# Kernel optimization log

Measured on AMD Instinct MI355X. Metric: run time of the kernel, lower is better.

The kernel has to match this reference:

```python
import jax, jax.numpy as jnp
import numpy as np

S, D, DD, REL, R = 4096, 128, 64, 8, 512
FC_IN = DD * (REL * S + R)  # 2,129,920


def setup_inputs() -> dict:
    key = jax.random.key(0)
    ks = jax.random.split(key, 7)
    return {
        "inputs": jax.random.randint(ks[0], (S,), 0, 2, dtype=jnp.int32),
        "rule_features": jax.random.normal(ks[1], (DD, R), dtype=jnp.float32),
        "embed_w": jax.random.normal(ks[2], (S, D), dtype=jnp.float32),
        "rel_w": jax.random.normal(ks[3], (REL, D), dtype=jnp.float32),
        "dise_w": jax.random.normal(ks[4], (DD, D), dtype=jnp.float32),
        "fc_w": jax.random.normal(ks[5], (DD, FC_IN), dtype=jnp.float32) * 0.01,
        "fc_b": jax.random.normal(ks[6], (DD,), dtype=jnp.float32),
    }


def reference(inputs, rule_features, embed_w, rel_w, dise_w, fc_w, fc_b):
    eps = 1e-6
    dt = embed_w.dtype
    # mask rows where the symptom indicator is nonzero (original builds mask
    # row-by-row with torch.nonzero; equivalent to broadcasting inputs != 0)
    mask = (inputs != 0).astype(dt)                                  # [S]
    # (embed + rel) * mask  -> [S, REL, D] -> [S*REL, D]
    x = (embed_w[:, None, :] + rel_w[None, :, :]) * mask[:, None, None]
    x = x.reshape(-1, embed_w.shape[-1])                             # [N, D]
    # cosine similarity of every disease embedding vs every (sym,rel) vector
    sq = jnp.sum(x * x, axis=1)                                      # [N]
    xn = jnp.where(sq > 0, jnp.sqrt(jnp.where(sq > 0, sq, 1.0)), 0.0)
    dn = jnp.sqrt(jnp.sum(dise_w * dise_w, axis=1))                  # [DD]
    dots = jnp.einsum('kd,nd->kn', dise_w, x)                        # [DD, N]
    kg = dots / jnp.maximum(dn[:, None] * xn[None, :], eps)          # [DD, N]
    hidden = jnp.concatenate([rule_features, kg], axis=1).reshape(1, -1)
    out = jax.nn.sigmoid(hidden @ fc_w.T + fc_b)                     # [1, DD]
    return out
```

## Files before the change

kernel.cpp:

```cpp
#include <hip/hip_runtime.h>
#include <math.h>

namespace {
constexpr int S_N   = 4096;
constexpr int D_N   = 128;
constexpr int DD_N  = 64;
constexpr int REL_N = 8;
constexpr int R_N   = 512;
constexpr int NTOT  = S_N * REL_N;
constexpr int ROWLEN = R_N + NTOT;
constexpr long long FC_IN_N = (long long)DD_N * ROWLEN;
constexpr int NCH   = 32;
constexpr int CHUNK2 = (int)(FC_IN_N / NCH);
constexpr int RPB   = 4;
constexpr int KG_N  = DD_N / RPB;
constexpr int NBLK3 = NCH * KG_N;
typedef float floatx4 __attribute__((ext_vector_type(4)));

__device__ __forceinline__ float dot4(const float4& a, const float4& b) {
    return a.x*b.x + a.y*b.y + a.z*b.z + a.w*b.w;
}
}

__global__ __launch_bounds__(256) void k_pre1(const float* __restrict__ dise,
                                              const float* __restrict__ embed,
                                              const float* __restrict__ rel,
                                              float* __restrict__ DE,
                                              float* __restrict__ DR,
                                              float* __restrict__ dsc_g) {
    __shared__ float sd[DD_N * 129];
    __shared__ __align__(16) float se[64 * D_N];
    __shared__ __align__(16) float sr[REL_N * D_N];
    const int tid  = threadIdx.x;
    const int lane = tid & 63;
    const int wave = tid >> 6;
    const int s0   = blockIdx.x * 64;

    for (int i = tid; i < DD_N * D_N; i += 256)
        sd[(i >> 7) * 129 + (i & 127)] = dise[i];
    for (int i = tid; i < 64 * D_N / 4; i += 256)
        reinterpret_cast<float4*>(se)[i] =
            reinterpret_cast<const float4*>(embed + (size_t)s0 * D_N)[i];
    if (tid < REL_N * D_N / 4)
        reinterpret_cast<float4*>(sr)[tid] = reinterpret_cast<const float4*>(rel)[tid];
    __syncthreads();

    float dw[D_N];
    float dsq = 0.f;
    #pragma unroll
    for (int e = 0; e < D_N; ++e) {
        dw[e] = sd[lane * 129 + e];
        dsq += dw[e] * dw[e];
    }
    const float dsc = rsqrtf(dsq);

    if (blockIdx.x == 0) {
        if (wave == 0) dsc_g[lane] = dsc;
        #pragma unroll
        for (int rr = 0; rr < 2; ++rr) {
            const int r = wave * 2 + rr;
            float a = 0.f;
            #pragma unroll
            for (int e = 0; e < D_N; ++e) a += dw[e] * sr[r * D_N + e];
            DR[lane * REL_N + r] = a;
        }
    }

    float* dst = DE + (size_t)lane * S_N + s0 + wave * 16;
    #pragma unroll
    for (int j4 = 0; j4 < 4; ++j4) {
        float4 o;
        float* op = reinterpret_cast<float*>(&o);
        #pragma unroll
        for (int jj = 0; jj < 4; ++jj) {
            const int nl = wave * 16 + j4 * 4 + jj;
            const float4* xr = reinterpret_cast<const float4*>(&se[nl * D_N]);
            float a0 = 0.f, a1 = 0.f, a2 = 0.f, a3 = 0.f;
            #pragma unroll
            for (int i = 0; i < 32; i += 4) {
                float4 x0 = xr[i], x1 = xr[i + 1], x2 = xr[i + 2], x3 = xr[i + 3];
                a0 += dw[4*i+ 0]*x0.x + dw[4*i+ 1]*x0.y + dw[4*i+ 2]*x0.z + dw[4*i+ 3]*x0.w;
                a1 += dw[4*i+ 4]*x1.x + dw[4*i+ 5]*x1.y + dw[4*i+ 6]*x1.z + dw[4*i+ 7]*x1.w;
                a2 += dw[4*i+ 8]*x2.x + dw[4*i+ 9]*x2.y + dw[4*i+10]*x2.z + dw[4*i+11]*x2.w;
                a3 += dw[4*i+12]*x3.x + dw[4*i+13]*x3.y + dw[4*i+14]*x3.z + dw[4*i+15]*x3.w;
            }
            op[jj] = a0 + a1 + a2 + a3;
        }
        *reinterpret_cast<float4*>(dst + j4 * 4) = o;
    }
}

__global__ __launch_bounds__(256) void k_pre0(const int* __restrict__ inputs,
                                              const float* __restrict__ embed,
                                              const float* __restrict__ rel,
                                              float* __restrict__ xinv) {
    __shared__ __align__(16) float sr[REL_N * D_N];
    __shared__ float rr[REL_N];
    const int tid = threadIdx.x;
    const int p  = tid & 3;
    const int sl = tid >> 2;
    const int s  = blockIdx.x * 64 + sl;

    if (tid < REL_N * D_N / 4)
        reinterpret_cast<float4*>(sr)[tid] = reinterpret_cast<const float4*>(rel)[tid];
    __syncthreads();
    if (tid < REL_N) {
        float a = 0.f;
        for (int e = 0; e < D_N; ++e) { float v = sr[tid * D_N + e]; a += v * v; }
        rr[tid] = a;
    }
    __syncthreads();

    float4 e4[8];
    const float4* ep = reinterpret_cast<const float4*>(embed + (size_t)s * D_N + p * 32);
    #pragma unroll
    for (int i = 0; i < 8; ++i) e4[i] = ep[i];
    float ee = 0.f;
    #pragma unroll
    for (int i = 0; i < 8; ++i) ee += dot4(e4[i], e4[i]);

    const float4* sr4 = reinterpret_cast<const float4*>(sr);
    float er[8];
    #pragma unroll
    for (int r = 0; r < REL_N; ++r) {
        float a = 0.f;
        #pragma unroll
        for (int i = 0; i < 8; ++i) a += dot4(e4[i], sr4[r * 32 + p * 8 + i]);
        er[r] = a;
    }

    ee += __shfl_xor(ee, 1); ee += __shfl_xor(ee, 2);
    #pragma unroll
    for (int r = 0; r < REL_N; ++r) {
        er[r] += __shfl_xor(er[r], 1);
        er[r] += __shfl_xor(er[r], 2);
    }

    if (p == 0) {
        const bool m = (inputs[s] != 0);
        float vr[8];
        #pragma unroll
        for (int r = 0; r < REL_N; ++r) {
            float sq = ee + 2.f * er[r] + rr[r];
            vr[r] = (m && sq > 0.f) ? rsqrtf(sq) : 0.f;
        }
        float4 o0, o1;
        o0.x = vr[0]; o0.y = vr[1]; o0.z = vr[2]; o0.w = vr[3];
        o1.x = vr[4]; o1.y = vr[5]; o1.z = vr[6]; o1.w = vr[7];
        float4* xp = reinterpret_cast<float4*>(xinv + (size_t)s * REL_N);
        xp[0] = o0; xp[1] = o1;
    }
}

__global__ __launch_bounds__(256) void k_kg2(const float* __restrict__ rf,
                                             const float* __restrict__ DE,
                                             const float* __restrict__ DR,
                                             const float* __restrict__ dsc_g,
                                             const float* __restrict__ xinv,
                                             float* __restrict__ h) {
    __shared__ __align__(16) float sx[8192];
    __shared__ float sD[1024];
    const int tid = threadIdx.x;
    const int dd  = blockIdx.x >> 2;
    const int q   = blockIdx.x & 3;
    const int n0  = q * 8192;
    const int s0  = q * 1024;

    for (int i = tid; i < 2048; i += 256)
        reinterpret_cast<float4*>(sx)[i] = reinterpret_cast<const float4*>(xinv + n0)[i];
    if (tid < 256)
        reinterpret_cast<float4*>(sD)[tid] =
            reinterpret_cast<const float4*>(DE + (size_t)dd * S_N + s0)[tid];
    const float dsc = dsc_g[dd];
    const float4 drlo = reinterpret_cast<const float4*>(DR + dd * REL_N)[0];
    const float4 drhi = reinterpret_cast<const float4*>(DR + dd * REL_N)[1];
    const float4 drv = (tid & 1) ? drhi : drlo;
    __syncthreads();

    float* hb = h + (size_t)dd * ROWLEN + R_N + n0;
    #pragma unroll
    for (int i = 0; i < 8; ++i) {
        const int f4i = i * 256 + tid;
        const int ln  = f4i * 4;
        const float de = sD[f4i >> 1];
        float4 xv = reinterpret_cast<const float4*>(sx)[f4i];
        float4 o;
        o.x = dsc * xv.x * (de + drv.x);
        o.y = dsc * xv.y * (de + drv.y);
        o.z = dsc * xv.z * (de + drv.z);
        o.w = dsc * xv.w * (de + drv.w);
        *reinterpret_cast<float4*>(hb + ln) = o;
    }
    if (q == 0 && tid < 128)
        reinterpret_cast<float4*>(h + (size_t)dd * ROWLEN)[tid] =
            reinterpret_cast<const float4*>(rf + (size_t)dd * R_N)[tid];
}

__global__ __launch_bounds__(256, 2) void k_mv(const float* __restrict__ fcw,
                                               const float* __restrict__ h,
                                               float* __restrict__ partials) {
    const int tid = threadIdx.x;
    const int swz = (blockIdx.x & 7) * (NBLK3 / 8) + (blockIdx.x >> 3);
    const int c  = swz >> 4;
    const int kg = swz & 15;

    const float4* hp = reinterpret_cast<const float4*>(h) + (size_t)c * (CHUNK2 / 4);
    const size_t wbase = (size_t)(kg * RPB) * (FC_IN_N / 4) + (size_t)c * (CHUNK2 / 4);
    const floatx4* wp0 = reinterpret_cast<const floatx4*>(fcw) + wbase;
    const floatx4* wp1 = wp0 + (FC_IN_N / 4);
    const floatx4* wp2 = wp1 + (FC_IN_N / 4);
    const floatx4* wp3 = wp2 + (FC_IN_N / 4);

    float a0 = 0.f, a1 = 0.f, a2 = 0.f, a3 = 0.f;
    #pragma unroll 5
    for (int i = 0; i < CHUNK2 / 4 / 256; ++i) {
        const int idx = i * 256 + tid;
        floatx4 w0 = __builtin_nontemporal_load(wp0 + idx);
        floatx4 w1 = __builtin_nontemporal_load(wp1 + idx);
        floatx4 w2 = __builtin_nontemporal_load(wp2 + idx);
        floatx4 w3 = __builtin_nontemporal_load(wp3 + idx);
        float4 hv = hp[idx];
        a0 += w0.x * hv.x + w0.y * hv.y + w0.z * hv.z + w0.w * hv.w;
        a1 += w1.x * hv.x + w1.y * hv.y + w1.z * hv.z + w1.w * hv.w;
        a2 += w2.x * hv.x + w2.y * hv.y + w2.z * hv.z + w2.w * hv.w;
        a3 += w3.x * hv.x + w3.y * hv.y + w3.z * hv.z + w3.w * hv.w;
    }

    #pragma unroll
    for (int m = 32; m >= 1; m >>= 1) {
        a0 += __shfl_xor(a0, m);
        a1 += __shfl_xor(a1, m);
        a2 += __shfl_xor(a2, m);
        a3 += __shfl_xor(a3, m);
    }
    __shared__ float red[4][RPB];
    if ((tid & 63) == 0) {
        const int wv = tid >> 6;
        red[wv][0] = a0; red[wv][1] = a1; red[wv][2] = a2; red[wv][3] = a3;
    }
    __syncthreads();
    if (tid < RPB) {
        partials[(size_t)swz * RPB + tid] =
            red[0][tid] + red[1][tid] + red[2][tid] + red[3][tid];
    }
}

__global__ __launch_bounds__(256) void k_fin(const float* __restrict__ partials,
                                             const float* __restrict__ fcb,
                                             float* __restrict__ out) {
    const int tid = threadIdx.x;
    const int k = tid & 63, g = tid >> 6;
    float s = 0.f;
    for (int b = g; b < NCH; b += 4) s += partials[(size_t)b * 64 + k];
    __shared__ float red[4][64];
    red[g][k] = s;
    __syncthreads();
    if (tid < 64) {
        float t = red[0][tid] + red[1][tid] + red[2][tid] + red[3][tid] + fcb[tid];
        out[tid] = 1.0f / (1.0f + expf(-t));
    }
}

extern "C" void kernel_launch(void* const* d_in, const int* in_sizes, int n_in,
                              void* d_out, int out_size, void* d_ws, size_t ws_size,
                              hipStream_t stream) {
    const int*   inputs = (const int*)  d_in[0];
    const float* rf     = (const float*)d_in[1];
    const float* embed  = (const float*)d_in[2];
    const float* rel    = (const float*)d_in[3];
    const float* dise   = (const float*)d_in[4];
    const float* fcw    = (const float*)d_in[5];
    const float* fcb    = (const float*)d_in[6];
    float* out = (float*)d_out;

    float* ws = (float*)d_ws;
    float* h        = ws;
    float* partials = h + FC_IN_N;
    float* DE       = partials + NCH * 64;
    float* DR       = DE + (size_t)DD_N * S_N;
    float* dsc_g    = DR + DD_N * REL_N;
    float* xinv     = dsc_g + 64;

    hipLaunchKernelGGL(k_pre1, dim3(S_N / 64), dim3(256), 0, stream, dise, embed, rel, DE, DR, dsc_g);
    hipLaunchKernelGGL(k_pre0, dim3(S_N / 64), dim3(256), 0, stream, inputs, embed, rel, xinv);
    hipLaunchKernelGGL(k_kg2,  dim3(DD_N * 4), dim3(256), 0, stream, rf, DE, DR, dsc_g, xinv, h);
    hipLaunchKernelGGL(k_mv,   dim3(NBLK3),    dim3(256), 0, stream, fcw, h, partials);
    hipLaunchKernelGGL(k_fin,  dim3(1),        dim3(256), 0, stream, partials, fcb, out);
}
```

Measured before the change: 117.9 us.

## Fuse preprocessing kernels and widen matvec blocks to eight rows

Merges the two preprocessing kernels into one that computes both the disease-embedding dot products and the inverse norms from the same shared tile. It uses 16 symptoms per block, giving four times as many blocks, and pads the shared rows to avoid bank conflicts. The fc matvec now uses 512-thread blocks that each handle 8 output rows, so every h load is reused across twice as many weight rows and there are half as many blocks. The trade-off is higher register pressure and fewer resident blocks in the dominant bandwidth-bound kernel, which could reduce memory-level parallelism.

```diff
diff --git a/kernel.cpp b/kernel.cpp
--- a/kernel.cpp
+++ b/kernel.cpp
@@ -12,9 +12,11 @@
 constexpr long long FC_IN_N = (long long)DD_N * ROWLEN;
 constexpr int NCH   = 32;
 constexpr int CHUNK2 = (int)(FC_IN_N / NCH);
-constexpr int RPB   = 4;
+constexpr int NF4   = CHUNK2 / 4;
+constexpr int RPB   = 8;
 constexpr int KG_N  = DD_N / RPB;
 constexpr int NBLK3 = NCH * KG_N;
+constexpr int SEP   = 132;
 typedef float floatx4 __attribute__((ext_vector_type(4)));
 
 __device__ __forceinline__ float dot4(const float4& a, const float4& b) {
@@ -22,28 +24,42 @@
 }
 }
 
-__global__ __launch_bounds__(256) void k_pre1(const float* __restrict__ dise,
-                                              const float* __restrict__ embed,
-                                              const float* __restrict__ rel,
-                                              float* __restrict__ DE,
-                                              float* __restrict__ DR,
-                                              float* __restrict__ dsc_g) {
+__global__ __launch_bounds__(256) void k_pre(const int* __restrict__ inputs,
+                                             const float* __restrict__ dise,
+                                             const float* __restrict__ embed,
+                                             const float* __restrict__ rel,
+                                             float* __restrict__ DE,
+                                             float* __restrict__ DR,
+                                             float* __restrict__ dsc_g,
+                                             float* __restrict__ xinv) {
     __shared__ float sd[DD_N * 129];
-    __shared__ __align__(16) float se[64 * D_N];
-    __shared__ __align__(16) float sr[REL_N * D_N];
+    __shared__ __align__(16) float se[16 * SEP];
+    __shared__ __align__(16) float sr[REL_N * SEP];
+    __shared__ float rr[REL_N];
     const int tid  = threadIdx.x;
     const int lane = tid & 63;
     const int wave = tid >> 6;
-    const int s0   = blockIdx.x * 64;
+    const int s0   = blockIdx.x * 16;
 
     for (int i = tid; i < DD_N * D_N; i += 256)
         sd[(i >> 7) * 129 + (i & 127)] = dise[i];
-    for (int i = tid; i < 64 * D_N / 4; i += 256)
-        reinterpret_cast<float4*>(se)[i] =
+    for (int i = tid; i < 16 * 32; i += 256) {
+        const int row = i >> 5, col = i & 31;
+        *reinterpret_cast<float4*>(&se[row * SEP + col * 4]) =
             reinterpret_cast<const float4*>(embed + (size_t)s0 * D_N)[i];
-    if (tid < REL_N * D_N / 4)
-        reinterpret_cast<float4*>(sr)[tid] = reinterpret_cast<const float4*>(rel)[tid];
-    __syncthreads();
+    }
+    if (tid < REL_N * 32) {
+        const int row = tid >> 5, col = tid & 31;
+        *reinterpret_cast<float4*>(&sr[row * SEP + col * 4]) =
+            reinterpret_cast<const float4*>(rel)[tid];
+    }
+    __syncthreads();
+
+    if (tid < REL_N) {
+        float a = 0.f;
+        for (int e = 0; e < D_N; ++e) { float v = sr[tid * SEP + e]; a += v * v; }
+        rr[tid] = a;
+    }
 
     float dw[D_N];
     float dsq = 0.f;
@@ -57,24 +73,22 @@
     if (blockIdx.x == 0) {
         if (wave == 0) dsc_g[lane] = dsc;
         #pragma unroll
-        for (int rr = 0; rr < 2; ++rr) {
-            const int r = wave * 2 + rr;
+        for (int rr2 = 0; rr2 < 2; ++rr2) {
+            const int r = wave * 2 + rr2;
             float a = 0.f;
             #pragma unroll
-            for (int e = 0; e < D_N; ++e) a += dw[e] * sr[r * D_N + e];
+            for (int e = 0; e < D_N; ++e) a += dw[e] * sr[r * SEP + e];
             DR[lane * REL_N + r] = a;
         }
     }
 
-    float* dst = DE + (size_t)lane * S_N + s0 + wave * 16;
-    #pragma unroll
-    for (int j4 = 0; j4 < 4; ++j4) {
+    {
         float4 o;
         float* op = reinterpret_cast<float*>(&o);
         #pragma unroll
         for (int jj = 0; jj < 4; ++jj) {
-            const int nl = wave * 16 + j4 * 4 + jj;
-            const float4* xr = reinterpret_cast<const float4*>(&se[nl * D_N]);
+            const int nl = wave * 4 + jj;
+            const float4* xr = reinterpret_cast<const float4*>(&se[nl * SEP]);
             float a0 = 0.f, a1 = 0.f, a2 = 0.f, a3 = 0.f;
             #pragma unroll
             for (int i = 0; i < 32; i += 4) {
@@ -86,69 +100,25 @@
             }
             op[jj] = a0 + a1 + a2 + a3;
         }
-        *reinterpret_cast<float4*>(dst + j4 * 4) = o;
-    }
-}
-
-__global__ __launch_bounds__(256) void k_pre0(const int* __restrict__ inputs,
-                                              const float* __restrict__ embed,
-                                              const float* __restrict__ rel,
-                                              float* __restrict__ xinv) {
-    __shared__ __align__(16) float sr[REL_N * D_N];
-    __shared__ float rr[REL_N];
-    const int tid = threadIdx.x;
-    const int p  = tid & 3;
-    const int sl = tid >> 2;
-    const int s  = blockIdx.x * 64 + sl;
-
-    if (tid < REL_N * D_N / 4)
-        reinterpret_cast<float4*>(sr)[tid] = reinterpret_cast<const float4*>(rel)[tid];
-    __syncthreads();
-    if (tid < REL_N) {
-        float a = 0.f;
-        for (int e = 0; e < D_N; ++e) { float v = sr[tid * D_N + e]; a += v * v; }
-        rr[tid] = a;
-    }
-    __syncthreads();
-
-    float4 e4[8];
-    const float4* ep = reinterpret_cast<const float4*>(embed + (size_t)s * D_N + p * 32);
-    #pragma unroll
-    for (int i = 0; i < 8; ++i) e4[i] = ep[i];
-    float ee = 0.f;
-    #pragma unroll
-    for (int i = 0; i < 8; ++i) ee += dot4(e4[i], e4[i]);
-
-    const float4* sr4 = reinterpret_cast<const float4*>(sr);
-    float er[8];
-    #pragma unroll
-    for (int r = 0; r < REL_N; ++r) {
-        float a = 0.f;
-        #pragma unroll
-        for (int i = 0; i < 8; ++i) a += dot4(e4[i], sr4[r * 32 + p * 8 + i]);
-        er[r] = a;
-    }
-
-    ee += __shfl_xor(ee, 1); ee += __shfl_xor(ee, 2);
-    #pragma unroll
-    for (int r = 0; r < REL_N; ++r) {
-        er[r] += __shfl_xor(er[r], 1);
-        er[r] += __shfl_xor(er[r], 2);
-    }
-
-    if (p == 0) {
-        const bool m = (inputs[s] != 0);
-        float vr[8];
-        #pragma unroll
-        for (int r = 0; r < REL_N; ++r) {
-            float sq = ee + 2.f * er[r] + rr[r];
-            vr[r] = (m && sq > 0.f) ? rsqrtf(sq) : 0.f;
-        }
-        float4 o0, o1;
-        o0.x = vr[0]; o0.y = vr[1]; o0.z = vr[2]; o0.w = vr[3];
-        o1.x = vr[4]; o1.y = vr[5]; o1.z = vr[6]; o1.w = vr[7];
-        float4* xp = reinterpret_cast<float4*>(xinv + (size_t)s * REL_N);
-        xp[0] = o0; xp[1] = o1;
+        *reinterpret_cast<float4*>(DE + (size_t)lane * S_N + s0 + wave * 4) = o;
+    }
+
+    __syncthreads();
+
+    if (tid < 128) {
+        const int sl = tid >> 3, r = tid & 7;
+        const float4* ev4 = reinterpret_cast<const float4*>(&se[sl * SEP]);
+        const float4* rv4 = reinterpret_cast<const float4*>(&sr[r * SEP]);
+        float ee = 0.f, er = 0.f;
+        #pragma unroll
+        for (int i = 0; i < 32; ++i) {
+            float4 ev = ev4[i], rv = rv4[i];
+            ee += dot4(ev, ev);
+            er += dot4(ev, rv);
+        }
+        const float sq = ee + 2.f * er + rr[r];
+        const bool m = (inputs[s0 + sl] != 0);
+        xinv[(size_t)(s0 + sl) * REL_N + r] = (m && sq > 0.f) ? rsqrtf(sq) : 0.f;
     }
 }
 
@@ -196,52 +166,59 @@
             reinterpret_cast<const float4*>(rf + (size_t)dd * R_N)[tid];
 }
 
-__global__ __launch_bounds__(256, 2) void k_mv(const float* __restrict__ fcw,
+__global__ __launch_bounds__(512, 1) void k_mv(const float* __restrict__ fcw,
                                                const float* __restrict__ h,
                                                float* __restrict__ partials) {
     const int tid = threadIdx.x;
     const int swz = (blockIdx.x & 7) * (NBLK3 / 8) + (blockIdx.x >> 3);
-    const int c  = swz >> 4;
-    const int kg = swz & 15;
-
-    const float4* hp = reinterpret_cast<const float4*>(h) + (size_t)c * (CHUNK2 / 4);
-    const size_t wbase = (size_t)(kg * RPB) * (FC_IN_N / 4) + (size_t)c * (CHUNK2 / 4);
-    const floatx4* wp0 = reinterpret_cast<const floatx4*>(fcw) + wbase;
-    const floatx4* wp1 = wp0 + (FC_IN_N / 4);
-    const floatx4* wp2 = wp1 + (FC_IN_N / 4);
-    const floatx4* wp3 = wp2 + (FC_IN_N / 4);
-
-    float a0 = 0.f, a1 = 0.f, a2 = 0.f, a3 = 0.f;
-    #pragma unroll 5
-    for (int i = 0; i < CHUNK2 / 4 / 256; ++i) {
-        const int idx = i * 256 + tid;
-        floatx4 w0 = __builtin_nontemporal_load(wp0 + idx);
-        floatx4 w1 = __builtin_nontemporal_load(wp1 + idx);
-        floatx4 w2 = __builtin_nontemporal_load(wp2 + idx);
-        floatx4 w3 = __builtin_nontemporal_load(wp3 + idx);
+    const int c  = swz >> 3;
+    const int kg = swz & 7;
+
+    const float4* hp = reinterpret_cast<const float4*>(h) + (size_t)c * NF4;
+    const floatx4* wp = reinterpret_cast<const floatx4*>(fcw)
+                        + (size_t)(kg * RPB) * (FC_IN_N / 4) + (size_t)c * NF4;
+
+    float acc[RPB];
+    #pragma unroll
+    for (int j = 0; j < RPB; ++j) acc[j] = 0.f;
+
+    #pragma unroll 2
+    for (int i = 0; i < 32; ++i) {
+        const int idx = i * 512 + tid;
         float4 hv = hp[idx];
-        a0 += w0.x * hv.x + w0.y * hv.y + w0.z * hv.z + w0.w * hv.w;
-        a1 += w1.x * hv.x + w1.y * hv.y + w1.z * hv.z + w1.w * hv.w;
-        a2 += w2.x * hv.x + w2.y * hv.y + w2.z * hv.z + w2.w * hv.w;
-        a3 += w3.x * hv.x + w3.y * hv.y + w3.z * hv.z + w3.w * hv.w;
+        #pragma unroll
+        for (int j = 0; j < RPB; ++j) {
+            floatx4 w = __builtin_nontemporal_load(wp + (size_t)j * (FC_IN_N / 4) + idx);
+            acc[j] += w.x * hv.x + w.y * hv.y + w.z * hv.z + w.w * hv.w;
+        }
+    }
+    if (tid < 256) {
+        const int idx = 32 * 512 + tid;
+        float4 hv = hp[idx];
+        #pragma unroll
+        for (int j = 0; j < RPB; ++j) {
+            floatx4 w = __builtin_nontemporal_load(wp + (size_t)j * (FC_IN_N / 4) + idx);
+            acc[j] += w.x * hv.x + w.y * hv.y + w.z * hv.z + w.w * hv.w;
+        }
     }
 
     #pragma unroll
     for (int m = 32; m >= 1; m >>= 1) {
-        a0 += __shfl_xor(a0, m);
-        a1 += __shfl_xor(a1, m);
-        a2 += __shfl_xor(a2, m);
-        a3 += __shfl_xor(a3, m);
-    }
-    __shared__ float red[4][RPB];
+        #pragma unroll
+        for (int j = 0; j < RPB; ++j) acc[j] += __shfl_xor(acc[j], m);
+    }
+    __shared__ float red[8][RPB];
     if ((tid & 63) == 0) {
         const int wv = tid >> 6;
-        red[wv][0] = a0; red[wv][1] = a1; red[wv][2] = a2; red[wv][3] = a3;
+        #pragma unroll
+        for (int j = 0; j < RPB; ++j) red[wv][j] = acc[j];
     }
     __syncthreads();
     if (tid < RPB) {
-        partials[(size_t)swz * RPB + tid] =
-            red[0][tid] + red[1][tid] + red[2][tid] + red[3][tid];
+        float s = 0.f;
+        #pragma unroll
+        for (int wv = 0; wv < 8; ++wv) s += red[wv][tid];
+        partials[(size_t)swz * RPB + tid] = s;
     }
 }
 
@@ -281,9 +258,9 @@
     float* dsc_g    = DR + DD_N * REL_N;
     float* xinv     = dsc_g + 64;
 
-    hipLaunchKernelGGL(k_pre1, dim3(S_N / 64), dim3(256), 0, stream, dise, embed, rel, DE, DR, dsc_g);
-    hipLaunchKernelGGL(k_pre0, dim3(S_N / 64), dim3(256), 0, stream, inputs, embed, rel, xinv);
+    hipLaunchKernelGGL(k_pre,  dim3(S_N / 16), dim3(256), 0, stream,
+                       inputs, dise, embed, rel, DE, DR, dsc_g, xinv);
     hipLaunchKernelGGL(k_kg2,  dim3(DD_N * 4), dim3(256), 0, stream, rf, DE, DR, dsc_g, xinv, h);
-    hipLaunchKernelGGL(k_mv,   dim3(NBLK3),    dim3(256), 0, stream, fcw, h, partials);
+    hipLaunchKernelGGL(k_mv,   dim3(NBLK3),    dim3(512), 0, stream, fcw, h, partials);
     hipLaunchKernelGGL(k_fin,  dim3(1),        dim3(256), 0, stream, partials, fcb, out);
 }
```

After: 112.1 us. 5.0% less time.
